# Kernel optimization log

Measured on AMD Instinct MI355X. Metric: run time of the kernel, lower is better.

The kernel has to match this reference:

```python
import jax, jax.numpy as jnp
import numpy as np
import math

D_MODEL = 1024
N_HEADS = 16
D_K = D_MODEL // N_HEADS
ROPE_BASE = 10000.0


def rope_cos_sin(seq_len, d_k, base=ROPE_BASE, dtype=jnp.float32):
    inv_freq = 1.0 / base ** (jnp.arange(0, d_k, 2, dtype=dtype) / d_k)  # [d_k/2]
    pos = jnp.arange(seq_len, dtype=dtype)
    freqs = jnp.outer(pos, inv_freq)  # [T, d_k/2]
    return jnp.cos(freqs), jnp.sin(freqs)


def apply_rope(x, cos, sin):
    # x: [B, H, T, d_k]; cos/sin: [T, d_k/2]
    x1 = x[..., 0::2]
    x2 = x[..., 1::2]
    c = cos[None, None]
    s = sin[None, None]
    r1 = x1 * c - x2 * s
    r2 = x1 * s + x2 * c
    return jnp.stack([r1, r2], axis=-1).reshape(x.shape)


def setup_inputs() -> dict:
    key = jax.random.key(0)
    ks = jax.random.split(key, 7)
    B, T = 2, 2048
    scale = 1.0 / math.sqrt(D_MODEL)
    return {
        "query": jax.random.normal(ks[0], (B, T, D_MODEL), jnp.float32),
        "key": jax.random.normal(ks[1], (B, T, D_MODEL), jnp.float32),
        "value": jax.random.normal(ks[2], (B, T, D_MODEL), jnp.float32),
        "Wq": jax.random.normal(ks[3], (D_MODEL, D_MODEL), jnp.float32) * scale,
        "Wk": jax.random.normal(ks[4], (D_MODEL, D_MODEL), jnp.float32) * scale,
        "Wv": jax.random.normal(ks[5], (D_MODEL, D_MODEL), jnp.float32) * scale,
        "Wo": jax.random.normal(ks[6], (D_MODEL, D_MODEL), jnp.float32) * scale,
    }


def reference(query, key, value, Wq, Wk, Wv, Wo):
    B, Tq, _ = query.shape
    Tk = key.shape[1]
    # nn.Linear: x @ W.T
    Q = (query @ Wq.T).reshape(B, Tq, N_HEADS, D_K).transpose(0, 2, 1, 3)
    K = (key @ Wk.T).reshape(B, Tk, N_HEADS, D_K).transpose(0, 2, 1, 3)
    V = (value @ Wv.T).reshape(B, Tk, N_HEADS, D_K).transpose(0, 2, 1, 3)
    cos_q, sin_q = rope_cos_sin(Tq, D_K)
    cos_k, sin_k = rope_cos_sin(Tk, D_K)
    Q = apply_rope(Q, cos_q, sin_q)
    K = apply_rope(K, cos_k, sin_k)
    scores = jnp.einsum("bhqd,bhkd->bhqk", Q, K) / math.sqrt(D_K)
    attn = jax.nn.softmax(scores, axis=-1)
    out = jnp.einsum("bhqk,bhkd->bhqd", attn, V)
    out = out.transpose(0, 2, 1, 3).reshape(B, Tq, D_MODEL)
    return out @ Wo.T
```

## Files before the change

### kernel.cpp

```cpp
#include <hip/hip_runtime.h>
#include <hip/hip_bf16.h>
#include <cstdint>

typedef unsigned short u16;
typedef __attribute__((ext_vector_type(4))) float fl4;
typedef __attribute__((ext_vector_type(2))) float fl2;
typedef __attribute__((ext_vector_type(4))) unsigned short u16x4;
typedef __attribute__((ext_vector_type(8))) unsigned short u16x8;
typedef __attribute__((ext_vector_type(2))) unsigned int u32x2;
typedef __attribute__((ext_vector_type(8))) __bf16 bf16x8;
typedef __attribute__((ext_vector_type(4))) float f32x4;

#define MKE 4194304
#define NKE 1048576

static __device__ __forceinline__ u16 f2bf(float x) {
  unsigned int u = __builtin_bit_cast(unsigned int, x);
  u += 0x7fffu + ((u >> 16) & 1u);
  return (u16)(u >> 16);
}

static __device__ __forceinline__ unsigned int cvtpk(float a, float b) {
  unsigned int r;
  asm("v_cvt_pk_bf16_f32 %0, %1, %2" : "=v"(r) : "v"(a), "v"(b));
  return r;
}

static __device__ __forceinline__ f32x4 mfma16(bf16x8 a, bf16x8 b, f32x4 c) {
  return __builtin_amdgcn_mfma_f32_16x16x32_bf16(a, b, c, 0, 0, 0);
}

static __device__ __forceinline__ void gload_lds16(const void* g, void* l) {
  __builtin_amdgcn_global_load_lds((const __attribute__((address_space(1))) void*)g,
                                   (__attribute__((address_space(3))) void*)l,
                                   16, 0, 0);
}

__global__ __launch_bounds__(256) void k_prep(const float* __restrict__ q,
                                              const float* __restrict__ k,
                                              const float* __restrict__ v,
                                              const float* __restrict__ wq,
                                              const float* __restrict__ wk,
                                              const float* __restrict__ wv,
                                              const float* __restrict__ wo,
                                              u16* __restrict__ ws,
                                              float* __restrict__ tab) {
  const int bid = blockIdx.x;
  if (bid >= 16384) {
    const int idx = (bid - 16384) * 256 + threadIdx.x;
    const int t = idx >> 5, i = idx & 31;
    const float ang = (float)t * exp2f(-0.4152410118609203f * (float)i);
    float sn, cs;
    sincosf(ang, &sn, &cs);
    reinterpret_cast<fl2*>(tab)[idx] = (fl2){cs, sn};
    return;
  }
  const int i = bid * 256 + threadIdx.x;
  const float* src;
  u16* dst;
  int loc;
  if (i < 3 * 1048576) {
    const int seg = i >> 20;
    loc = i & 1048575;
    src = seg == 0 ? q : (seg == 1 ? k : v);
    dst = ws + (size_t)seg * MKE;
  } else {
    const int j = i - 3 * 1048576;
    const int seg = j >> 18;
    loc = j & 262143;
    src = seg == 0 ? wq : (seg == 1 ? wk : (seg == 2 ? wv : wo));
    dst = ws + 3 * (size_t)MKE + (size_t)seg * NKE;
  }
  fl4 val = reinterpret_cast<const fl4*>(src)[loc];
  u16x4 o;
  o[0] = f2bf(val[0]); o[1] = f2bf(val[1]); o[2] = f2bf(val[2]); o[3] = f2bf(val[3]);
  reinterpret_cast<u16x4*>(dst)[loc] = o;
}

__global__ __launch_bounds__(256) void k_gemm_qkv(
    const u16* __restrict__ aq, const u16* __restrict__ ak, const u16* __restrict__ av,
    const u16* __restrict__ bq, const u16* __restrict__ bk, const u16* __restrict__ bv,
    u16* __restrict__ cq, u16* __restrict__ ck, u16* __restrict__ cv,
    const fl2* __restrict__ tab) {
  constexpr int K = 1024;
  __shared__ __align__(16) u16 smem[16384];
  u16* sA = smem;
  u16* sB = smem + 8192;
  const int z = blockIdx.z;
  const u16* A  = z == 0 ? aq : (z == 1 ? ak : av);
  const u16* Bw = z == 0 ? bq : (z == 1 ? bk : bv);
  u16* C        = z == 0 ? cq : (z == 1 ? ck : cv);
  const float scale = (z == 0) ? 0.18033688011112042f : 1.0f;

  const int tid = threadIdx.x;
  const int w = tid >> 6, lane = tid & 63;
  const int wm = w >> 1, wn = w & 1;
  const int trow = blockIdx.y << 7, tcol = blockIdx.x << 7;
  const int l15 = lane & 15, l4 = lane >> 4;
  const int srow = lane >> 3;
  const int scol = ((lane & 7) ^ srow) << 3;

  f32x4 acc[4][4];
#pragma unroll
  for (int m = 0; m < 4; ++m)
#pragma unroll
    for (int n = 0; n < 4; ++n) acc[m][n] = (f32x4){0.f, 0.f, 0.f, 0.f};

  for (int k0 = 0; k0 < K; k0 += 64) {
#pragma unroll
    for (int c = 0; c < 4; ++c) {
      const int g = c * 4 + w;
      const int row = g * 8 + srow;
      gload_lds16(A + (size_t)(trow + row) * K + (k0 + scol), (void*)(sA + g * 512));
      gload_lds16(Bw + (size_t)(tcol + row) * K + (k0 + scol), (void*)(sB + g * 512));
    }
    __syncthreads();
#pragma unroll
    for (int kc = 0; kc < 2; ++kc) {
      const int kb = (kc * 32 + l4 * 8) * 2;
      bf16x8 af[4], bfr[4];
#pragma unroll
      for (int m = 0; m < 4; ++m) {
        const int r = wm * 64 + m * 16 + l15;
        af[m] = *reinterpret_cast<const bf16x8*>(
            reinterpret_cast<const char*>(sA) + r * 128 + (kb ^ ((r & 7) << 4)));
      }
#pragma unroll
      for (int n = 0; n < 4; ++n) {
        const int r = wn * 64 + n * 16 + l15;
        bfr[n] = *reinterpret_cast<const bf16x8*>(
            reinterpret_cast<const char*>(sB) + r * 128 + (kb ^ ((r & 7) << 4)));
      }
      __builtin_amdgcn_s_setprio(1);
#pragma unroll
      for (int m = 0; m < 4; ++m)
#pragma unroll
        for (int n = 0; n < 4; ++n)
          acc[m][n] = mfma16(af[m], bfr[n], acc[m][n]);
      __builtin_amdgcn_s_setprio(0);
    }
    __syncthreads();
  }

  if (z < 2) {
#pragma unroll
    for (int m = 0; m < 4; ++m) {
#pragma unroll
      for (int n = 0; n < 4; ++n) {
#pragma unroll
        for (int r = 0; r < 4; ++r) {
          const float vsc = acc[m][n][r] * scale;
          const int row = trow + wm * 64 + m * 16 + l4 * 4 + r;
          const int col = tcol + wn * 64 + n * 16 + l15;
          const int b = row >> 11, t = row & 2047;
          const int h = col >> 6, d = col & 63;
          const float partner = __shfl_xor(vsc, 1);
          const fl2 cs = tab[t * 32 + (d >> 1)];
          const float outv =
              (d & 1) ? (partner * cs.y + vsc * cs.x) : (vsc * cs.x - partner * cs.y);
          C[((size_t)((b << 4) + h) * 2048 + t) * 64 + d] = f2bf(outv);
        }
      }
    }
  } else {
#pragma unroll
    for (int m = 0; m < 4; ++m)
#pragma unroll
      for (int n = 0; n < 4; ++n)
#pragma unroll
        for (int r = 0; r < 4; ++r) {
          const int c = wn * 64 + n * 16 + l15;
          const int rl = wm * 64 + m * 16 + l4 * 4 + r;
          smem[c * 128 + (rl ^ ((c & 15) * 8))] = f2bf(acc[m][n][r]);
        }
    __syncthreads();
    const int bq = trow >> 11;
    const int tb = trow & 2047;
#pragma unroll
    for (int j = 0; j < 8; ++j) {
      const int flat = (tid + j * 256) * 8;
      const int c = flat >> 7, r0 = flat & 127;
      u16x8 vv = *reinterpret_cast<const u16x8*>(smem + c * 128 + (r0 ^ ((c & 15) * 8)));
      const int col = tcol + c;
      u16* dst = C + ((size_t)((bq << 4) + (col >> 6)) * 64 + (col & 63)) * 2048 + tb + r0;
      *reinterpret_cast<u16x8*>(dst) = vv;
    }
  }
}

__global__ __launch_bounds__(256) void k_gemm_o(const u16* __restrict__ A,
                                                const u16* __restrict__ Bw,
                                                float* __restrict__ C) {
  constexpr int K = 1024, N = 1024;
  __shared__ __align__(16) u16 sA[2][128 * 64];
  __shared__ __align__(16) u16 sB[2][64 * 64];
  const int tid = threadIdx.x;
  const int w = tid >> 6, lane = tid & 63;
  const int wm = w >> 1, wn = w & 1;
  const int trow = blockIdx.y << 7, tcol = blockIdx.x << 6;
  const int l15 = lane & 15, l4 = lane >> 4;
  const int srow = lane >> 3;
  const int scol = ((lane & 7) ^ srow) << 3;

  f32x4 acc[4][2];
#pragma unroll
  for (int m = 0; m < 4; ++m)
#pragma unroll
    for (int n = 0; n < 2; ++n) acc[m][n] = (f32x4){0.f, 0.f, 0.f, 0.f};

  auto stage = [&](int k0, int buf) {
#pragma unroll
    for (int c = 0; c < 4; ++c) {
      const int g = c * 4 + w;
      const int row = g * 8 + srow;
      gload_lds16(A + (size_t)(trow + row) * K + (k0 + scol), (void*)(sA[buf] + g * 512));
    }
#pragma unroll
    for (int c = 0; c < 2; ++c) {
      const int g = c * 4 + w;
      const int row = g * 8 + srow;
      gload_lds16(Bw + (size_t)(tcol + row) * K + (k0 + scol), (void*)(sB[buf] + g * 512));
    }
  };

  stage(0, 0);
  __syncthreads();

  for (int t = 0; t < 16; ++t) {
    const int buf = t & 1;
    if (t + 1 < 16) stage((t + 1) * 64, buf ^ 1);
#pragma unroll
    for (int kc = 0; kc < 2; ++kc) {
      const int kb = (kc * 32 + l4 * 8) * 2;
      bf16x8 af[4], bfr[2];
#pragma unroll
      for (int m = 0; m < 4; ++m) {
        const int r = wm * 64 + m * 16 + l15;
        af[m] = *reinterpret_cast<const bf16x8*>(
            reinterpret_cast<const char*>(sA[buf]) + r * 128 + (kb ^ ((r & 7) << 4)));
      }
#pragma unroll
      for (int n = 0; n < 2; ++n) {
        const int r = wn * 32 + n * 16 + l15;
        bfr[n] = *reinterpret_cast<const bf16x8*>(
            reinterpret_cast<const char*>(sB[buf]) + r * 128 + (kb ^ ((r & 7) << 4)));
      }
      __builtin_amdgcn_s_setprio(1);
#pragma unroll
      for (int m = 0; m < 4; ++m)
#pragma unroll
        for (int n = 0; n < 2; ++n)
          acc[m][n] = mfma16(af[m], bfr[n], acc[m][n]);
      __builtin_amdgcn_s_setprio(0);
    }
    __syncthreads();
  }

#pragma unroll
  for (int m = 0; m < 4; ++m)
#pragma unroll
    for (int n = 0; n < 2; ++n)
#pragma unroll
      for (int r = 0; r < 4; ++r) {
        const int row = trow + wm * 64 + m * 16 + l4 * 4 + r;
        const int col = tcol + wn * 32 + n * 16 + l15;
        C[(size_t)row * N + col] = acc[m][n][r];
      }
}

__global__ __launch_bounds__(256) void k_attn(const u16* __restrict__ Q,
                                              const u16* __restrict__ Kh,
                                              const u16* __restrict__ Vt,
                                              u16* __restrict__ Oout) {
  __shared__ __align__(16) char lds[49152];
  const int tid = threadIdx.x;
  const int w = tid >> 6, lane = tid & 63;
  const int l15 = lane & 15, l4 = lane >> 4;
  const int nb = blockIdx.x;
  const int xcd = nb & 7, idx = nb >> 3;
  const int bh = xcd * 4 + (idx >> 4);
  const int q0 = (idx & 15) << 7;

  const u16* Qg = Q + (size_t)bh * (2048 * 64);
  const u16* Kg = Kh + (size_t)bh * (2048 * 64);
  const u16* Vg = Vt + (size_t)bh * (64 * 2048);

  const int swz = (l15 & 7) << 4;
  const int rk0 = l15 * 128 + ((l4 * 16) ^ swz);
  const int rk1 = rk0 ^ 64;
  const int pbase = 32768 + w * 4096 + l15 * 128;
  int pwvA[4];
#pragma unroll
  for (int nn = 0; nn < 4; ++nn) pwvA[nn] = pbase + (((nn * 32) | (l4 * 8)) ^ swz);
  const int rpA0 = pbase + ((l4 * 16) ^ swz);
  const int rpA1 = rpA0 ^ 64;
  const int wst = w * 1024;

  const int srow8 = lane >> 3;
  const int scol = ((lane & 7) ^ srow8) << 3;
  const u16* gK0 = Kg + (size_t)(w * 8 + srow8) * 64 + scol;
  const u16* gK1 = gK0 + 2048;
  const u16* gV0 = Vg + (size_t)(w * 8 + srow8) * 2048 + scol;
  const u16* gV1 = gV0 + 65536;

  bf16x8 qf0, qf1, qf2, qf3;
  {
    const u16* qpA = Qg + (size_t)(q0 + w * 32 + l15) * 64 + l4 * 8;
    qf0 = *reinterpret_cast<const bf16x8*>(qpA);
    qf1 = *reinterpret_cast<const bf16x8*>(qpA + 32);
    const u16* qpB = qpA + 16 * 64;
    qf2 = *reinterpret_cast<const bf16x8*>(qpB);
    qf3 = *reinterpret_cast<const bf16x8*>(qpB + 32);
  }

  f32x4 oA[4], oB[4];
#pragma unroll
  for (int nn = 0; nn < 4; ++nn) {
    oA[nn] = (f32x4){0.f, 0.f, 0.f, 0.f};
    oB[nn] = (f32x4){0.f, 0.f, 0.f, 0.f};
  }
  float lrunA = 0.f, lrunB = 0.f;

  gload_lds16(gK0, lds + wst);
  gload_lds16(gK1, lds + wst + 4096);
  gload_lds16(gV0, lds + 16384 + wst);
  gload_lds16(gV1, lds + 16384 + wst + 4096);
  gK0 += 4096; gK1 += 4096; gV0 += 64; gV1 += 64;
  __syncthreads();

#define ATTN_STEP(BUFOFF, PREF, POFF)                                            \
  {                                                                              \
    if (PREF) {                                                                  \
      gload_lds16(gK0, lds + (POFF) + wst);                                      \
      gload_lds16(gK1, lds + (POFF) + wst + 4096);                               \
      gload_lds16(gV0, lds + 16384 + (POFF) + wst);                              \
      gload_lds16(gV1, lds + 16384 + (POFF) + wst + 4096);                       \
      gK0 += 4096; gK1 += 4096; gV0 += 64; gV1 += 64;                            \
    }                                                                            \
    f32x4 sA[4], sB[4];                                                          \
    __builtin_amdgcn_s_setprio(1);                                               \
    _Pragma("unroll")                                                            \
    for (int nn = 0; nn < 4; ++nn) {                                             \
      bf16x8 kf = *(const bf16x8*)(lds + (BUFOFF) + rk0 + nn * 2048);            \
      sA[nn] = mfma16(kf, qf0, (f32x4){0.f, 0.f, 0.f, 0.f});                     \
      sB[nn] = mfma16(kf, qf2, (f32x4){0.f, 0.f, 0.f, 0.f});                     \
    }                                                                            \
    _Pragma("unroll")                                                            \
    for (int nn = 0; nn < 4; ++nn) {                                             \
      bf16x8 kf = *(const bf16x8*)(lds + (BUFOFF) + rk1 + nn * 2048);            \
      sA[nn] = mfma16(kf, qf1, sA[nn]);                                          \
      sB[nn] = mfma16(kf, qf3, sB[nn]);                                          \
    }                                                                            \
    __builtin_amdgcn_s_setprio(0);                                               \
    float ppA[4][4], ppB[4][4];                                                  \
    _Pragma("unroll")                                                            \
    for (int nn = 0; nn < 4; ++nn) {                                             \
      ppA[nn][0] = __builtin_amdgcn_exp2f(sA[nn][0]);                            \
      ppA[nn][1] = __builtin_amdgcn_exp2f(sA[nn][1]);                            \
      ppA[nn][2] = __builtin_amdgcn_exp2f(sA[nn][2]);                            \
      ppA[nn][3] = __builtin_amdgcn_exp2f(sA[nn][3]);                            \
      ppB[nn][0] = __builtin_amdgcn_exp2f(sB[nn][0]);                            \
      ppB[nn][1] = __builtin_amdgcn_exp2f(sB[nn][1]);                            \
      ppB[nn][2] = __builtin_amdgcn_exp2f(sB[nn][2]);                            \
      ppB[nn][3] = __builtin_amdgcn_exp2f(sB[nn][3]);                            \
    }                                                                            \
    _Pragma("unroll")                                                            \
    for (int nn = 0; nn < 4; ++nn) {                                             \
      u32x2 pkA, pkB;                                                            \
      pkA[0] = cvtpk(ppA[nn][0], ppA[nn][1]);                                    \
      pkA[1] = cvtpk(ppA[nn][2], ppA[nn][3]);                                    \
      pkB[0] = cvtpk(ppB[nn][0], ppB[nn][1]);                                    \
      pkB[1] = cvtpk(ppB[nn][2], ppB[nn][3]);                                    \
      *(u32x2*)(lds + pwvA[nn]) = pkA;                                           \
      *(u32x2*)(lds + pwvA[nn] + 2048) = pkB;                                    \
    }                                                                            \
    float rsA = ((ppA[0][0] + ppA[0][1]) + (ppA[0][2] + ppA[0][3])) +            \
                ((ppA[1][0] + ppA[1][1]) + (ppA[1][2] + ppA[1][3])) +            \
                ((ppA[2][0] + ppA[2][1]) + (ppA[2][2] + ppA[2][3])) +            \
                ((ppA[3][0] + ppA[3][1]) + (ppA[3][2] + ppA[3][3]));             \
    float rsB = ((ppB[0][0] + ppB[0][1]) + (ppB[0][2] + ppB[0][3])) +            \
                ((ppB[1][0] + ppB[1][1]) + (ppB[1][2] + ppB[1][3])) +            \
                ((ppB[2][0] + ppB[2][1]) + (ppB[2][2] + ppB[2][3])) +            \
                ((ppB[3][0] + ppB[3][1]) + (ppB[3][2] + ppB[3][3]));             \
    rsA += __shfl_xor(rsA, 16);                                                  \
    rsA += __shfl_xor(rsA, 32);                                                  \
    rsB += __shfl_xor(rsB, 16);                                                  \
    rsB += __shfl_xor(rsB, 32);                                                  \
    lrunA += rsA;                                                                \
    lrunB += rsB;                                                                \
    __builtin_amdgcn_s_setprio(1);                                               \
    _Pragma("unroll")                                                            \
    for (int kc = 0; kc < 2; ++kc) {                                             \
      const bf16x8 pfA = *(const bf16x8*)(lds + (kc ? rpA1 : rpA0));             \
      const bf16x8 pfB = *(const bf16x8*)(lds + (kc ? rpA1 : rpA0) + 2048);      \
      const int rkk = kc ? rk1 : rk0;                                            \
      _Pragma("unroll")                                                          \
      for (int nn = 0; nn < 4; ++nn) {                                           \
        bf16x8 vf = *(const bf16x8*)(lds + 16384 + (BUFOFF) + rkk + nn * 2048);  \
        oA[nn] = mfma16(pfA, vf, oA[nn]);                                        \
        oB[nn] = mfma16(pfB, vf, oB[nn]);                                        \
      }                                                                          \
    }                                                                            \
    __builtin_amdgcn_s_setprio(0);                                               \
    __syncthreads();                                                             \
  }

  for (int cc = 0; cc < 16; ++cc) {
    ATTN_STEP(0, 1, 8192)
    ATTN_STEP(8192, (cc != 15), 0)
  }
#undef ATTN_STEP

  const int b = bh >> 4, h = bh & 15;
  float lrA[4], lrB[4];
#pragma unroll
  for (int r = 0; r < 4; ++r) {
    const int src = (lane & 48) | (l4 * 4 + r);
    lrA[r] = 1.f / __shfl(lrunA, src);
    lrB[r] = 1.f / __shfl(lrunB, src);
  }
#pragma unroll
  for (int nn = 0; nn < 4; ++nn)
#pragma unroll
    for (int r = 0; r < 4; ++r) {
      const int tA = q0 + w * 32 + l4 * 4 + r;
      const int d = nn * 16 + l15;
      Oout[((size_t)(b * 2048 + tA)) * 1024 + h * 64 + d] = f2bf(oA[nn][r] * lrA[r]);
      Oout[((size_t)(b * 2048 + tA + 16)) * 1024 + h * 64 + d] = f2bf(oB[nn][r] * lrB[r]);
    }
}

extern "C" void kernel_launch(void* const* d_in, const int* in_sizes, int n_in,
                              void* d_out, int out_size, void* d_ws, size_t ws_size,
                              hipStream_t stream) {
  const float* q  = (const float*)d_in[0];
  const float* k  = (const float*)d_in[1];
  const float* v  = (const float*)d_in[2];
  const float* wq = (const float*)d_in[3];
  const float* wk = (const float*)d_in[4];
  const float* wv = (const float*)d_in[5];
  const float* wo = (const float*)d_in[6];

  u16* ws = (u16*)d_ws;
  u16* Xq  = ws;
  u16* Xk  = Xq + MKE;
  u16* Xv  = Xk + MKE;
  u16* Wqb = Xv + MKE;
  u16* Wkb = Wqb + NKE;
  u16* Wvb = Wkb + NKE;
  u16* Wob = Wvb + NKE;
  u16* Qr  = Wob + NKE;
  u16* Kr  = Qr + MKE;
  u16* Vtm = Kr + MKE;
  u16* Vtr = Vtm + MKE;
  u16* AO  = Vtr + MKE;
  float* tab = (float*)AO;

  k_prep<<<16640, 256, 0, stream>>>(q, k, v, wq, wk, wv, wo, ws, tab);
  k_gemm_qkv<<<dim3(8, 32, 3), 256, 0, stream>>>(Xq, Xk, Xv, Wqb, Wkb, Wvb,
                                                 Qr, Kr, Vtr, (const fl2*)tab);
  k_attn<<<512, 256, 0, stream>>>(Qr, Kr, Vtr, AO);
  k_gemm_o<<<dim3(16, 32), 256, 0, stream>>>(AO, Wob, (float*)d_out);
}
```

Before: 129.9 us.

## Triple-buffer K/V tiles and compute next QK^T scores one step ahead

Moves K/V staging in the attention kernel from double to triple buffering with rotating buffer offsets. The kernel now computes the QK^T scores for the next tile before the softmax and PV work of the current tile. The goal is to overlap the matrix-core score computation with the exp, packing and PV phases, and to give global loads more lead time. In exchange LDS use grows from 48KB to 64KB per block, which can lower occupancy, and keeping two sets of score registers raises register pressure.

```diff
diff --git a/kernel.cpp b/kernel.cpp
--- a/kernel.cpp
+++ b/kernel.cpp
@@ -272,7 +272,7 @@
                                               const u16* __restrict__ Kh,
                                               const u16* __restrict__ Vt,
                                               u16* __restrict__ Oout) {
-  __shared__ __align__(16) char lds[49152];
+  __shared__ __align__(16) char lds[65536];
   const int tid = threadIdx.x;
   const int w = tid >> 6, lane = tid & 63;
   const int l15 = lane & 15, l4 = lane >> 4;
@@ -288,7 +288,7 @@
   const int swz = (l15 & 7) << 4;
   const int rk0 = l15 * 128 + ((l4 * 16) ^ swz);
   const int rk1 = rk0 ^ 64;
-  const int pbase = 32768 + w * 4096 + l15 * 128;
+  const int pbase = 49152 + w * 4096 + l15 * 128;
   int pwvA[4];
 #pragma unroll
   for (int nn = 0; nn < 4; ++nn) pwvA[nn] = pbase + (((nn * 32) | (l4 * 8)) ^ swz);
@@ -323,46 +323,70 @@
 
   gload_lds16(gK0, lds + wst);
   gload_lds16(gK1, lds + wst + 4096);
-  gload_lds16(gV0, lds + 16384 + wst);
-  gload_lds16(gV1, lds + 16384 + wst + 4096);
+  gload_lds16(gV0, lds + 24576 + wst);
+  gload_lds16(gV1, lds + 24576 + wst + 4096);
+  gK0 += 4096; gK1 += 4096; gV0 += 64; gV1 += 64;
+  gload_lds16(gK0, lds + 8192 + wst);
+  gload_lds16(gK1, lds + 8192 + wst + 4096);
+  gload_lds16(gV0, lds + 24576 + 8192 + wst);
+  gload_lds16(gV1, lds + 24576 + 8192 + wst + 4096);
   gK0 += 4096; gK1 += 4096; gV0 += 64; gV1 += 64;
   __syncthreads();
 
-#define ATTN_STEP(BUFOFF, PREF, POFF)                                            \
+  int bcur = 0, bnxt = 8192, bnn = 16384;
+
+  f32x4 s0A[4], s0B[4], s1A[4], s1B[4];
+  __builtin_amdgcn_s_setprio(1);
+#pragma unroll
+  for (int nn = 0; nn < 4; ++nn) {
+    bf16x8 kf = *(const bf16x8*)(lds + rk0 + nn * 2048);
+    s0A[nn] = mfma16(kf, qf0, (f32x4){0.f, 0.f, 0.f, 0.f});
+    s0B[nn] = mfma16(kf, qf2, (f32x4){0.f, 0.f, 0.f, 0.f});
+  }
+#pragma unroll
+  for (int nn = 0; nn < 4; ++nn) {
+    bf16x8 kf = *(const bf16x8*)(lds + rk1 + nn * 2048);
+    s0A[nn] = mfma16(kf, qf1, s0A[nn]);
+    s0B[nn] = mfma16(kf, qf3, s0B[nn]);
+  }
+  __builtin_amdgcn_s_setprio(0);
+
+#define ATTN_STEP(SCA, SCB, SNA, SNB, DO_STAGE, DO_QKT)                          \
   {                                                                              \
-    if (PREF) {                                                                  \
-      gload_lds16(gK0, lds + (POFF) + wst);                                      \
-      gload_lds16(gK1, lds + (POFF) + wst + 4096);                               \
-      gload_lds16(gV0, lds + 16384 + (POFF) + wst);                              \
-      gload_lds16(gV1, lds + 16384 + (POFF) + wst + 4096);                       \
+    if (DO_STAGE) {                                                              \
+      gload_lds16(gK0, lds + bnn + wst);                                         \
+      gload_lds16(gK1, lds + bnn + wst + 4096);                                  \
+      gload_lds16(gV0, lds + 24576 + bnn + wst);                                 \
+      gload_lds16(gV1, lds + 24576 + bnn + wst + 4096);                          \
       gK0 += 4096; gK1 += 4096; gV0 += 64; gV1 += 64;                            \
     }                                                                            \
-    f32x4 sA[4], sB[4];                                                          \
-    __builtin_amdgcn_s_setprio(1);                                               \
-    _Pragma("unroll")                                                            \
-    for (int nn = 0; nn < 4; ++nn) {                                             \
-      bf16x8 kf = *(const bf16x8*)(lds + (BUFOFF) + rk0 + nn * 2048);            \
-      sA[nn] = mfma16(kf, qf0, (f32x4){0.f, 0.f, 0.f, 0.f});                     \
-      sB[nn] = mfma16(kf, qf2, (f32x4){0.f, 0.f, 0.f, 0.f});                     \
+    if (DO_QKT) {                                                                \
+      __builtin_amdgcn_s_setprio(1);                                             \
+      _Pragma("unroll")                                                          \
+      for (int nn = 0; nn < 4; ++nn) {                                           \
+        bf16x8 kf = *(const bf16x8*)(lds + bnxt + rk0 + nn * 2048);              \
+        SNA[nn] = mfma16(kf, qf0, (f32x4){0.f, 0.f, 0.f, 0.f});                  \
+        SNB[nn] = mfma16(kf, qf2, (f32x4){0.f, 0.f, 0.f, 0.f});                  \
+      }                                                                          \
+      _Pragma("unroll")                                                          \
+      for (int nn = 0; nn < 4; ++nn) {                                           \
+        bf16x8 kf = *(const bf16x8*)(lds + bnxt + rk1 + nn * 2048);              \
+        SNA[nn] = mfma16(kf, qf1, SNA[nn]);                                      \
+        SNB[nn] = mfma16(kf, qf3, SNB[nn]);                                      \
+      }                                                                          \
+      __builtin_amdgcn_s_setprio(0);                                             \
     }                                                                            \
-    _Pragma("unroll")                                                            \
-    for (int nn = 0; nn < 4; ++nn) {                                             \
-      bf16x8 kf = *(const bf16x8*)(lds + (BUFOFF) + rk1 + nn * 2048);            \
-      sA[nn] = mfma16(kf, qf1, sA[nn]);                                          \
-      sB[nn] = mfma16(kf, qf3, sB[nn]);                                          \
-    }                                                                            \
-    __builtin_amdgcn_s_setprio(0);                                               \
     float ppA[4][4], ppB[4][4];                                                  \
     _Pragma("unroll")                                                            \
     for (int nn = 0; nn < 4; ++nn) {                                             \
-      ppA[nn][0] = __builtin_amdgcn_exp2f(sA[nn][0]);                            \
-      ppA[nn][1] = __builtin_amdgcn_exp2f(sA[nn][1]);                            \
-      ppA[nn][2] = __builtin_amdgcn_exp2f(sA[nn][2]);                            \
-      ppA[nn][3] = __builtin_amdgcn_exp2f(sA[nn][3]);                            \
-      ppB[nn][0] = __builtin_amdgcn_exp2f(sB[nn][0]);                            \
-      ppB[nn][1] = __builtin_amdgcn_exp2f(sB[nn][1]);                            \
-      ppB[nn][2] = __builtin_amdgcn_exp2f(sB[nn][2]);                            \
-      ppB[nn][3] = __builtin_amdgcn_exp2f(sB[nn][3]);                            \
+      ppA[nn][0] = __builtin_amdgcn_exp2f(SCA[nn][0]);                           \
+      ppA[nn][1] = __builtin_amdgcn_exp2f(SCA[nn][1]);                           \
+      ppA[nn][2] = __builtin_amdgcn_exp2f(SCA[nn][2]);                           \
+      ppA[nn][3] = __builtin_amdgcn_exp2f(SCA[nn][3]);                           \
+      ppB[nn][0] = __builtin_amdgcn_exp2f(SCB[nn][0]);                           \
+      ppB[nn][1] = __builtin_amdgcn_exp2f(SCB[nn][1]);                           \
+      ppB[nn][2] = __builtin_amdgcn_exp2f(SCB[nn][2]);                           \
+      ppB[nn][3] = __builtin_amdgcn_exp2f(SCB[nn][3]);                           \
     }                                                                            \
     _Pragma("unroll")                                                            \
     for (int nn = 0; nn < 4; ++nn) {                                             \
@@ -396,18 +420,20 @@
       const int rkk = kc ? rk1 : rk0;                                            \
       _Pragma("unroll")                                                          \
       for (int nn = 0; nn < 4; ++nn) {                                           \
-        bf16x8 vf = *(const bf16x8*)(lds + 16384 + (BUFOFF) + rkk + nn * 2048);  \
+        bf16x8 vf = *(const bf16x8*)(lds + 24576 + bcur + rkk + nn * 2048);      \
         oA[nn] = mfma16(pfA, vf, oA[nn]);                                        \
         oB[nn] = mfma16(pfB, vf, oB[nn]);                                        \
       }                                                                          \
     }                                                                            \
     __builtin_amdgcn_s_setprio(0);                                               \
     __syncthreads();                                                             \
+    { const int tmp = bcur; bcur = bnxt; bnxt = bnn; bnn = tmp; }                \
   }
 
   for (int cc = 0; cc < 16; ++cc) {
-    ATTN_STEP(0, 1, 8192)
-    ATTN_STEP(8192, (cc != 15), 0)
+    const bool st = (cc <= 14);
+    ATTN_STEP(s0A, s0B, s1A, s1B, st, true)
+    ATTN_STEP(s1A, s1B, s0A, s0B, st, st)
   }
 #undef ATTN_STEP
 
```

New measurement: 129.7 us. About the same (-0.1%).
